# Kernel optimization log

Hardware: AMD Instinct MI355X
Metric: run time of the kernel (lower is better)

Reference implementation:

```python
import jax, jax.numpy as jnp
import numpy as np

D_IN = 1024
D_OUT = 1024


def setup_inputs() -> dict:
    key = jax.random.key(0)
    kx, kq, kk, kv = jax.random.split(key, 4)
    B, T = 8, 2048
    x = jax.random.normal(kx, (B, T, D_IN), dtype=jnp.float32)
    # torch Linear weight is (d_out, d_in); we store transposed (d_in, d_out)
    s = 1.0 / np.sqrt(D_IN)
    Wq = jax.random.uniform(kq, (D_IN, D_OUT), jnp.float32, -s, s)
    Wk = jax.random.uniform(kk, (D_IN, D_OUT), jnp.float32, -s, s)
    Wv = jax.random.uniform(kv, (D_IN, D_OUT), jnp.float32, -s, s)
    return {"x": x, "Wq": Wq, "Wk": Wk, "Wv": Wv}


def reference(x, Wq, Wk, Wv):
    # x: (B, T, d_in)
    T = x.shape[1]
    d_out = Wq.shape[1]
    q = jnp.einsum('btd,de->bte', x, Wq)  # (B,T,d_out)
    k = jnp.einsum('btd,de->bte', x, Wk)
    v = jnp.einsum('btd,de->bte', x, Wv)
    scores = jnp.einsum('bqe,bke->bqk', q, k)  # (B,T,T)
    causal = jnp.tril(jnp.ones((T, T), dtype=bool))  # True = keep
    scores = jnp.where(causal[None], scores, -jnp.inf)
    weights = jax.nn.softmax(scores / jnp.sqrt(jnp.asarray(d_out, x.dtype)), axis=-1)
    # dropout p=0.0 -> identity
    return jnp.einsum('bqk,bke->bqe', weights, v)  # (B,T,d_out)
```

## Files before the change

### kernel.cpp

```cpp
#include <hip/hip_runtime.h>

using u16 = unsigned short;
typedef __bf16 bf16x8 __attribute__((ext_vector_type(8)));
typedef float floatx4 __attribute__((ext_vector_type(4)));

__device__ __forceinline__ u16 f2bf(float f) {
  union { float f; unsigned u; } c; c.f = f;
  unsigned u = c.u;
  u += 0x7fffu + ((u >> 16) & 1u);
  return (u16)(u >> 16);
}

__device__ __forceinline__ void st_out(float* p, float v) { *p = v; }
__device__ __forceinline__ void st_out(u16* p, float v) { *p = f2bf(v); }

__device__ __forceinline__ void load16(const u16* g, u16* l) {
  __builtin_amdgcn_global_load_lds(
      (const __attribute__((address_space(1))) void*)g,
      (__attribute__((address_space(3))) void*)l, 16, 0, 0);
}

#define TILE 128
#define BK 64

template<typename OutT>
__device__ __forceinline__ void gemm_core(
    const u16* __restrict__ A, int lda, long sA,
    const u16* __restrict__ Bt, int ldb, long sB,
    OutT* __restrict__ C, int ldc, long sC,
    int kmax, int bx, int by, int bz, int tid)
{
  __shared__ u16 As[TILE * BK];
  __shared__ u16 Bs[TILE * BK];

  const u16* Ab = A + bz * sA + (long)by * TILE * lda;
  const u16* Bb = Bt + bz * sB + (long)bx * TILE * ldb;

  int lane = tid & 63;
  int wm = ((tid >> 7) & 1) * 64;
  int wn = ((tid >> 6) & 1) * 64;

  floatx4 acc[4][4] = {};
  int arow = wm + (lane & 15);
  int brow = wn + (lane & 15);
  int q = lane >> 4;

  for (int k0 = 0; k0 < kmax; k0 += BK) {
    __syncthreads();
#pragma unroll
    for (int h = 0; h < 4; h++) {
      int cc = tid + h * 256;
      int row = cc >> 3, gm = (cc & 7) ^ (row & 7);
      load16(Ab + (long)row * lda + k0 + gm * 8, &As[cc * 8]);
    }
#pragma unroll
    for (int h = 0; h < 4; h++) {
      int cc = tid + h * 256;
      int row = cc >> 3, gm = (cc & 7) ^ (row & 7);
      load16(Bb + (long)row * ldb + k0 + gm * 8, &Bs[cc * 8]);
    }
    __builtin_amdgcn_s_waitcnt(0);
    __syncthreads();

#pragma unroll
    for (int kp = 0; kp < 2; kp++) {
      bf16x8 a[4], b[4];
#pragma unroll
      for (int i = 0; i < 4; i++) {
        int r = arow + i * 16;
        a[i] = *(const bf16x8*)&As[(r * 8 + ((kp * 4 + q) ^ (r & 7))) * 8];
      }
#pragma unroll
      for (int j = 0; j < 4; j++) {
        int r = brow + j * 16;
        b[j] = *(const bf16x8*)&Bs[(r * 8 + ((kp * 4 + q) ^ (r & 7))) * 8];
      }
#pragma unroll
      for (int i = 0; i < 4; i++)
#pragma unroll
        for (int j = 0; j < 4; j++)
          acc[i][j] = __builtin_amdgcn_mfma_f32_16x16x32_bf16(a[i], b[j], acc[i][j], 0, 0, 0);
    }
  }

  OutT* Cb = C + bz * sC;
  int colbase = bx * TILE + wn + (lane & 15);
  int rowbase = by * TILE + wm + ((lane >> 4) << 2);
#pragma unroll
  for (int i = 0; i < 4; i++)
#pragma unroll
    for (int j = 0; j < 4; j++) {
      int col = colbase + j * 16;
#pragma unroll
      for (int r = 0; r < 4; r++)
        st_out(&Cb[(long)(rowbase + i * 16 + r) * ldc + col], acc[i][j][r]);
    }
}

template<typename OutT>
__global__ __launch_bounds__(256, 2)
void gemm_rect(const u16* __restrict__ A, int lda, long sA,
               const u16* __restrict__ Bt, int ldb, long sB,
               OutT* __restrict__ C, int ldc, long sC, int K,
               int l2gx, int nO8s)
{
  int L = blockIdx.x;
  int t = ((L & 7) << nO8s) | (L >> 3);
  int bx = t & ((1 << l2gx) - 1), by = t >> l2gx;
  gemm_core<OutT>(A, lda, sA, Bt, ldb, sB, C, ldc, sC, K, bx, by, blockIdx.y, threadIdx.x);
}

__global__ __launch_bounds__(256, 2)
void gemm_tri(const u16* __restrict__ A, int lda, long sA,
              const u16* __restrict__ Bt, int ldb, long sB,
              float* __restrict__ C, int ldc, long sC, int K)
{
  int tp = blockIdx.x;
  int t = (tp & 7) * 17 + (tp >> 3);
  int r = (int)((sqrtf(8.f * t + 1.f) - 1.f) * 0.5f);
  while ((r + 1) * (r + 2) / 2 <= t) ++r;
  while (r * (r + 1) / 2 > t) --r;
  int c = t - r * (r + 1) / 2;
  gemm_core<float>(A, lda, sA, Bt, ldb, sB, C, ldc, sC, K, c, r, blockIdx.y, threadIdx.x);
}

__global__ __launch_bounds__(256, 2)
void gemm_opv(const u16* __restrict__ P, int lda, long sA,
              const u16* __restrict__ VT, int ldb, long sB,
              float* __restrict__ C, int ldc, long sC)
{
  int L = blockIdx.x;
  int j = L & 7, s = L >> 3;
  int by = (s < 8) ? j : 15 - j;
  int bx = s & 7;
  gemm_core<float>(P, lda, sA, VT, ldb, sB, C, ldc, sC,
                   (by + 1) * TILE, bx, by, blockIdx.y, threadIdx.x);
}

__global__ __launch_bounds__(256)
void cvt_x(const float4* __restrict__ x, u16* __restrict__ o, int n4)
{
  int i = blockIdx.x * 256 + threadIdx.x;
  if (i >= n4) return;
  float4 v = x[i];
  ushort4 r;
  r.x = f2bf(v.x); r.y = f2bf(v.y); r.z = f2bf(v.z); r.w = f2bf(v.w);
  *(ushort4*)(o + (long)i * 4) = r;
}

__global__ __launch_bounds__(256)
void cvt_w(const float* __restrict__ W, u16* __restrict__ O)
{
  const int D = 1024;
  __shared__ float t[64][65];
  int tid = threadIdx.x;
  int c = tid & 63, r = tid >> 6;
  int e0 = blockIdx.x * 64, d0 = blockIdx.y * 64;
  for (int rr = r; rr < 64; rr += 4)
    t[rr][c] = W[(long)(d0 + rr) * D + e0 + c];
  __syncthreads();
  for (int rr = r; rr < 64; rr += 4)
    O[(long)(e0 + rr) * D + d0 + c] = f2bf(t[c][rr]);
}

__global__ __launch_bounds__(256)
void softmax_causal(float* __restrict__ S, float scale)
{
  const int T = 2048;
  int row = blockIdx.x & (T - 1);
  int bi  = blockIdx.x >> 11;
  float* Srow = S + ((long)bi * T + row) * T;
  u16* Prow = (u16*)Srow;
  int n = row + 1;
  int nw = ((row >> 7) + 1) << 7;

  __shared__ float buf[T];
  __shared__ float red[8];
  int tid = threadIdx.x, lane = tid & 63, wid = tid >> 6;

  float lmax = -3.0e38f;
  for (int i = tid; i < n; i += 256) {
    float v = Srow[i] * scale;
    buf[i] = v;
    lmax = fmaxf(lmax, v);
  }
#pragma unroll
  for (int o = 32; o > 0; o >>= 1) lmax = fmaxf(lmax, __shfl_down(lmax, o, 64));
  if (lane == 0) red[wid] = lmax;
  __syncthreads();
  float m = fmaxf(fmaxf(red[0], red[1]), fmaxf(red[2], red[3]));

  float lsum = 0.f;
  for (int i = tid; i < n; i += 256) {
    float e = __expf(buf[i] - m);
    buf[i] = e;
    lsum += e;
  }
#pragma unroll
  for (int o = 32; o > 0; o >>= 1) lsum += __shfl_down(lsum, o, 64);
  if (lane == 0) red[4 + wid] = lsum;
  __syncthreads();
  float inv = 1.0f / (red[4] + red[5] + red[6] + red[7]);

  for (int i = tid; i < n; i += 256) Prow[i] = f2bf(buf[i] * inv);
  for (int i = n + tid; i < nw; i += 256) Prow[i] = 0;
}

extern "C" void kernel_launch(void* const* d_in, const int* in_sizes, int n_in,
                              void* d_out, int out_size, void* d_ws, size_t ws_size,
                              hipStream_t stream)
{
  const int B = 8, T = 2048, D = 1024;
  const float* x  = (const float*)d_in[0];
  const float* Wq = (const float*)d_in[1];
  const float* Wk = (const float*)d_in[2];
  const float* Wv = (const float*)d_in[3];
  float* out = (float*)d_out;
  char* ws = (char*)d_ws;

  const size_t OFF_X   = 0;
  const size_t OFF_WQ  = 32ul << 20;
  const size_t OFF_WK  = 34ul << 20;
  const size_t OFF_WVT = 36ul << 20;
  const size_t OFF_NT  = 38ul << 20;
  const size_t OFF_Y   = 40ul << 20;
  const size_t OFF_VT  = 72ul << 20;
  const size_t OFF_S   = 104ul << 20;

  u16* xb  = (u16*)(ws + OFF_X);
  u16* Wqb = (u16*)(ws + OFF_WQ);
  u16* Wkb = (u16*)(ws + OFF_WK);
  u16* WvT = (u16*)(ws + OFF_WVT);
  u16* NT  = (u16*)(ws + OFF_NT);
  u16* Yb  = (u16*)(ws + OFF_Y);
  u16* VT  = (u16*)(ws + OFF_VT);
  float* S = (float*)(ws + OFF_S);

  int NB = 8;
  while (NB > 1 && OFF_S + (size_t)NB * T * T * 4 > ws_size) NB >>= 1;

  cvt_x<<<(B * T * D / 4 + 255) / 256, 256, 0, stream>>>((const float4*)x, xb, B * T * D / 4);
  cvt_x<<<(D * D / 4 + 255) / 256, 256, 0, stream>>>((const float4*)Wq, Wqb, D * D / 4);
  cvt_x<<<(D * D / 4 + 255) / 256, 256, 0, stream>>>((const float4*)Wk, Wkb, D * D / 4);
  cvt_w<<<dim3(16, 16), 256, 0, stream>>>(Wv, WvT);

  gemm_rect<u16><<<dim3(64, 1), 256, 0, stream>>>(
      Wkb, D, 0L, Wqb, D, 0L, NT, D, 0L, D, 3, 3);
  gemm_rect<u16><<<dim3(1024, 1), 256, 0, stream>>>(
      xb, D, 0L, NT, D, 0L, Yb, D, 0L, D, 3, 7);
  gemm_rect<u16><<<dim3(1024, 1), 256, 0, stream>>>(
      WvT, D, 0L, xb, D, 0L, VT, B * T, 0L, D, 7, 7);

  for (int b0 = 0; b0 < B; b0 += NB) {
    gemm_tri<<<dim3(136, NB), 256, 0, stream>>>(
        Yb + (long)b0 * T * D, D, (long)T * D,
        xb + (long)b0 * T * D, D, (long)T * D,
        S, T, (long)T * T, D);
    softmax_causal<<<NB * T, 256, 0, stream>>>(S, 0.03125f);
    gemm_opv<<<dim3(128, NB), 256, 0, stream>>>(
        (const u16*)S, 2 * T, (long)T * 2 * T,
        VT + (long)b0 * T, B * T, (long)T,
        out + (long)b0 * T * D, D, (long)T * D);
  }
}
```

Baseline: 392.7 us.

## Store attention scores in bf16, fold scale into Wq, fuse projection GEMMs

The score GEMM now writes bf16 instead of fp32, which halves the traffic of the score matrix, and the softmax works in registers on 8-element vectors with no shared-memory buffer. The 1/sqrt(d) scale is folded into the Wq conversion. The Y and V projection GEMMs are merged into one launch of 2048 blocks, and the P·V block ordering is reversed so the heavy rows are scheduled first. The trade-off is lower precision in the scores before softmax, since bf16 rounding of the logits adds error. Wqb also aliases Yb's buffer, which relies on NT being computed before Yb is written.

```diff
diff --git a/kernel.cpp b/kernel.cpp
--- a/kernel.cpp
+++ b/kernel.cpp
@@ -2,6 +2,7 @@
 
 using u16 = unsigned short;
 typedef __bf16 bf16x8 __attribute__((ext_vector_type(8)));
+typedef unsigned short u16x8 __attribute__((ext_vector_type(8)));
 typedef float floatx4 __attribute__((ext_vector_type(4)));
 
 __device__ __forceinline__ u16 f2bf(float f) {
@@ -9,6 +10,9 @@
   unsigned u = c.u;
   u += 0x7fffu + ((u >> 16) & 1u);
   return (u16)(u >> 16);
+}
+__device__ __forceinline__ float bf2f(u16 h) {
+  union { unsigned u; float f; } c; c.u = ((unsigned)h) << 16; return c.f;
 }
 
 __device__ __forceinline__ void st_out(float* p, float v) { *p = v; }
@@ -111,9 +115,26 @@
 }
 
 __global__ __launch_bounds__(256, 2)
+void gemm_proj(const u16* __restrict__ xb, const u16* __restrict__ NT,
+               const u16* __restrict__ WvT, u16* __restrict__ Yb,
+               u16* __restrict__ VT)
+{
+  int L = blockIdx.x;
+  bool h = (L >= 1024);
+  int LL = h ? L - 1024 : L;
+  int t = ((LL & 7) << 7) | (LL >> 3);
+  int bx = h ? (t & 127) : (t & 7);
+  int by = h ? (t >> 7) : (t >> 3);
+  gemm_core<u16>(h ? WvT : xb, 1024, 0L,
+                 h ? xb : NT, 1024, 0L,
+                 h ? VT : Yb, h ? 16384 : 1024, 0L,
+                 1024, bx, by, 0, threadIdx.x);
+}
+
+__global__ __launch_bounds__(256, 2)
 void gemm_tri(const u16* __restrict__ A, int lda, long sA,
               const u16* __restrict__ Bt, int ldb, long sB,
-              float* __restrict__ C, int ldc, long sC, int K)
+              u16* __restrict__ C, int ldc, long sC, int K)
 {
   int tp = blockIdx.x;
   int t = (tp & 7) * 17 + (tp >> 3);
@@ -121,7 +142,7 @@
   while ((r + 1) * (r + 2) / 2 <= t) ++r;
   while (r * (r + 1) / 2 > t) --r;
   int c = t - r * (r + 1) / 2;
-  gemm_core<float>(A, lda, sA, Bt, ldb, sB, C, ldc, sC, K, c, r, blockIdx.y, threadIdx.x);
+  gemm_core<u16>(A, lda, sA, Bt, ldb, sB, C, ldc, sC, K, c, r, blockIdx.y, threadIdx.x);
 }
 
 __global__ __launch_bounds__(256, 2)
@@ -131,20 +152,21 @@
 {
   int L = blockIdx.x;
   int j = L & 7, s = L >> 3;
-  int by = (s < 8) ? j : 15 - j;
+  int by = (s < 8) ? 15 - j : j;
   int bx = s & 7;
   gemm_core<float>(P, lda, sA, VT, ldb, sB, C, ldc, sC,
                    (by + 1) * TILE, bx, by, blockIdx.y, threadIdx.x);
 }
 
 __global__ __launch_bounds__(256)
-void cvt_x(const float4* __restrict__ x, u16* __restrict__ o, int n4)
+void cvt_x(const float4* __restrict__ x, u16* __restrict__ o, int n4, float scale)
 {
   int i = blockIdx.x * 256 + threadIdx.x;
   if (i >= n4) return;
   float4 v = x[i];
   ushort4 r;
-  r.x = f2bf(v.x); r.y = f2bf(v.y); r.z = f2bf(v.z); r.w = f2bf(v.w);
+  r.x = f2bf(v.x * scale); r.y = f2bf(v.y * scale);
+  r.z = f2bf(v.z * scale); r.w = f2bf(v.w * scale);
   *(ushort4*)(o + (long)i * 4) = r;
 }
 
@@ -164,26 +186,24 @@
 }
 
 __global__ __launch_bounds__(256)
-void softmax_causal(float* __restrict__ S, float scale)
+void softmax_bf16(u16* __restrict__ S)
 {
   const int T = 2048;
   int row = blockIdx.x & (T - 1);
-  int bi  = blockIdx.x >> 11;
-  float* Srow = S + ((long)bi * T + row) * T;
-  u16* Prow = (u16*)Srow;
+  u16* Prow = S + (long)blockIdx.x * T;
   int n = row + 1;
-  int nw = ((row >> 7) + 1) << 7;
-
-  __shared__ float buf[T];
+  int tid = threadIdx.x, lane = tid & 63, wid = tid >> 6;
+  int i0 = tid * 8;
+
+  u16x8 pv = *(const u16x8*)(Prow + i0);
+  float v[8];
+  float lmax = -3.0e38f;
+#pragma unroll
+  for (int j = 0; j < 8; j++) {
+    v[j] = (i0 + j < n) ? bf2f(pv[j]) : -3.0e38f;
+    lmax = fmaxf(lmax, v[j]);
+  }
   __shared__ float red[8];
-  int tid = threadIdx.x, lane = tid & 63, wid = tid >> 6;
-
-  float lmax = -3.0e38f;
-  for (int i = tid; i < n; i += 256) {
-    float v = Srow[i] * scale;
-    buf[i] = v;
-    lmax = fmaxf(lmax, v);
-  }
 #pragma unroll
   for (int o = 32; o > 0; o >>= 1) lmax = fmaxf(lmax, __shfl_down(lmax, o, 64));
   if (lane == 0) red[wid] = lmax;
@@ -191,9 +211,10 @@
   float m = fmaxf(fmaxf(red[0], red[1]), fmaxf(red[2], red[3]));
 
   float lsum = 0.f;
-  for (int i = tid; i < n; i += 256) {
-    float e = __expf(buf[i] - m);
-    buf[i] = e;
+#pragma unroll
+  for (int j = 0; j < 8; j++) {
+    float e = (i0 + j < n) ? __expf(v[j] - m) : 0.f;
+    v[j] = e;
     lsum += e;
   }
 #pragma unroll
@@ -202,8 +223,10 @@
   __syncthreads();
   float inv = 1.0f / (red[4] + red[5] + red[6] + red[7]);
 
-  for (int i = tid; i < n; i += 256) Prow[i] = f2bf(buf[i] * inv);
-  for (int i = n + tid; i < nw; i += 256) Prow[i] = 0;
+  u16x8 w;
+#pragma unroll
+  for (int j = 0; j < 8; j++) w[j] = f2bf(v[j] * inv);
+  *(u16x8*)(Prow + i0) = w;
 }
 
 extern "C" void kernel_launch(void* const* d_in, const int* in_sizes, int n_in,
@@ -218,47 +241,36 @@
   float* out = (float*)d_out;
   char* ws = (char*)d_ws;
 
-  const size_t OFF_X   = 0;
-  const size_t OFF_WQ  = 32ul << 20;
-  const size_t OFF_WK  = 34ul << 20;
-  const size_t OFF_WVT = 36ul << 20;
-  const size_t OFF_NT  = 38ul << 20;
-  const size_t OFF_Y   = 40ul << 20;
-  const size_t OFF_VT  = 72ul << 20;
-  const size_t OFF_S   = 104ul << 20;
-
-  u16* xb  = (u16*)(ws + OFF_X);
-  u16* Wqb = (u16*)(ws + OFF_WQ);
-  u16* Wkb = (u16*)(ws + OFF_WK);
-  u16* WvT = (u16*)(ws + OFF_WVT);
-  u16* NT  = (u16*)(ws + OFF_NT);
-  u16* Yb  = (u16*)(ws + OFF_Y);
-  u16* VT  = (u16*)(ws + OFF_VT);
-  float* S = (float*)(ws + OFF_S);
-
+  u16* xb  = (u16*)(ws);
+  u16* WvT = (u16*)(ws + (32ul << 20));
+  u16* NT  = (u16*)(ws + (34ul << 20));
+  u16* Yb  = (u16*)(ws + (36ul << 20));
+  u16* Wqb = Yb;
+  u16* Wkb = (u16*)(ws + (38ul << 20));
+  u16* VT  = (u16*)(ws + (68ul << 20));
+  u16* S   = (u16*)(ws + (100ul << 20));
+
+  const size_t OFF_S = 100ul << 20;
   int NB = 8;
-  while (NB > 1 && OFF_S + (size_t)NB * T * T * 4 > ws_size) NB >>= 1;
-
-  cvt_x<<<(B * T * D / 4 + 255) / 256, 256, 0, stream>>>((const float4*)x, xb, B * T * D / 4);
-  cvt_x<<<(D * D / 4 + 255) / 256, 256, 0, stream>>>((const float4*)Wq, Wqb, D * D / 4);
-  cvt_x<<<(D * D / 4 + 255) / 256, 256, 0, stream>>>((const float4*)Wk, Wkb, D * D / 4);
+  while (NB > 1 && OFF_S + (size_t)NB * T * T * 2 > ws_size) NB >>= 1;
+
+  cvt_x<<<(B * T * D / 4 + 255) / 256, 256, 0, stream>>>((const float4*)x, xb, B * T * D / 4, 1.0f);
+  cvt_x<<<(D * D / 4 + 255) / 256, 256, 0, stream>>>((const float4*)Wq, Wqb, D * D / 4, 0.03125f);
+  cvt_x<<<(D * D / 4 + 255) / 256, 256, 0, stream>>>((const float4*)Wk, Wkb, D * D / 4, 1.0f);
   cvt_w<<<dim3(16, 16), 256, 0, stream>>>(Wv, WvT);
 
   gemm_rect<u16><<<dim3(64, 1), 256, 0, stream>>>(
       Wkb, D, 0L, Wqb, D, 0L, NT, D, 0L, D, 3, 3);
-  gemm_rect<u16><<<dim3(1024, 1), 256, 0, stream>>>(
-      xb, D, 0L, NT, D, 0L, Yb, D, 0L, D, 3, 7);
-  gemm_rect<u16><<<dim3(1024, 1), 256, 0, stream>>>(
-      WvT, D, 0L, xb, D, 0L, VT, B * T, 0L, D, 7, 7);
+  gemm_proj<<<dim3(2048, 1), 256, 0, stream>>>(xb, NT, WvT, Yb, VT);
 
   for (int b0 = 0; b0 < B; b0 += NB) {
     gemm_tri<<<dim3(136, NB), 256, 0, stream>>>(
         Yb + (long)b0 * T * D, D, (long)T * D,
         xb + (long)b0 * T * D, D, (long)T * D,
         S, T, (long)T * T, D);
-    softmax_causal<<<NB * T, 256, 0, stream>>>(S, 0.03125f);
+    softmax_bf16<<<NB * T, 256, 0, stream>>>(S);
     gemm_opv<<<dim3(128, NB), 256, 0, stream>>>(
-        (const u16*)S, 2 * T, (long)T * 2 * T,
+        S, T, (long)T * T,
         VT + (long)b0 * T, B * T, (long)T,
         out + (long)b0 * T * D, D, (long)T * D);
   }
```

Result: faster. 370.2 us (-5.7%).
